# Optimization experiments

Hardware: AMD Instinct MI355X
Metric: run time of the kernel (lower is better)

Reference implementation:

```python
import jax, jax.numpy as jnp
import numpy as np

# dims: B=32 batch, F=40 max_frames, NB=36 num_boxes, R=512 region size, H=512 hidden
# feat_size D = R + 2H = 1536 ; relation attn input = 2D = 3072

def _soft_attention(feats, hidden, Wf, bf, Wh, bh, wa):
    # feats: (N, L, Din), hidden: (N, H) -> att feat (N, Din), alpha (N, L)
    e = jnp.tanh(feats @ Wf.T + bf + (hidden @ Wh.T + bh)[:, None, :]) @ wa  # (N, L)
    alpha = jax.nn.softmax(e, axis=1)
    att = jnp.einsum('nl,nld->nd', alpha, feats)
    return att, alpha


def setup_inputs() -> dict:
    key = jax.random.key(0)
    ks = jax.random.split(key, 16)
    B, F, NB, R, H = 32, 40, 36, 512, 512
    D = R + 2 * H  # 1536
    s = 0.02
    inp = {
        'i3d_feats': jax.random.normal(ks[0], (B, F, 2 * H), jnp.float32),
        'object_feats': jax.random.normal(ks[1], (B, F, NB, R), jnp.float32),
        'hidden_state': jax.random.normal(ks[2], (B, H), jnp.float32),
        # spatial SoftAttention(R, H, H)
        'Ws_f': jax.random.normal(ks[3], (H, R), jnp.float32) * s,
        'bs_f': jnp.zeros((H,), jnp.float32),
        'Ws_h': jax.random.normal(ks[4], (H, H), jnp.float32) * s,
        'bs_h': jnp.zeros((H,), jnp.float32),
        'was': jax.random.normal(ks[5], (H,), jnp.float32) * s,
        # relation SoftAttention(2D, H, H)
        'Wr_f': jax.random.normal(ks[6], (H, 2 * D), jnp.float32) * s,
        'br_f': jnp.zeros((H,), jnp.float32),
        'Wr_h': jax.random.normal(ks[7], (H, H), jnp.float32) * s,
        'br_h': jnp.zeros((H,), jnp.float32),
        'war': jax.random.normal(ks[8], (H,), jnp.float32) * s,
    }
    return inp


def reference(i3d_feats, object_feats, hidden_state,
              Ws_f, bs_f, Ws_h, bs_h, was,
              Wr_f, br_f, Wr_h, br_h, war):
    B, F, NB, R = object_feats.shape
    # ---- spatial attention over boxes (per frame) ----
    feats = object_feats.reshape(B * F, NB, R)
    hidden_rep = jnp.repeat(hidden_state, F, axis=0)  # == hidden.repeat(1,F).reshape(B*F,-1)
    obj_att, _ = _soft_attention(feats, hidden_rep, Ws_f, bs_f, Ws_h, bs_h, was)
    obj_att = obj_att.reshape(B, F, R)
    feat = jnp.concatenate([obj_att, i3d_feats], axis=-1)  # (B, F, D)
    D = feat.shape[-1]
    # ---- relation attention over all F*F frame pairs ----
    # pairwise[b, i*F + j] = concat(feat[b, j], feat[b, i])  (feat1 varies fast, feat2 slow)
    # Decompose Wr_f @ concat(fj, fi) = Wr1 @ fj + Wr2 @ fi to avoid O(F^2 * 2D) tensor.
    Wr1, Wr2 = Wr_f[:, :D], Wr_f[:, D:]
    p1 = feat @ Wr1.T  # (B, F, H), applied to fast index j
    p2 = feat @ Wr2.T  # (B, F, H), applied to slow index i
    hproj = hidden_state @ Wr_h.T + br_h  # (B, H)
    e = jnp.tanh(p2[:, :, None, :] + p1[:, None, :, :] + (hproj + br_f)[:, None, None, :]) @ war  # (B,F,F) [i,j]
    alpha = jax.nn.softmax(e.reshape(B, F * F), axis=1).reshape(B, F, F)
    # weighted sum of concat(feat[j], feat[i]) splits into two marginal sums
    rel1 = jnp.einsum('bij,bjd->bd', alpha, feat)
    rel2 = jnp.einsum('bij,bid->bd', alpha, feat)
    return jnp.concatenate([rel1, rel2], axis=-1)  # (B, 2D)
```

## Files before the change

### kernel.cpp

```cpp
#include <hip/hip_runtime.h>
#include <stdint.h>

#define B_SZ 32
#define F_SZ 40
#define NB_SZ 36
#define R_SZ 512
#define H_SZ 512
#define D_SZ 1536
#define M1 (B_SZ * F_SZ * NB_SZ)
#define NROW (B_SZ * F_SZ)
#define FNB (F_SZ * NB_SZ)

typedef __attribute__((ext_vector_type(8))) short short8;
typedef __attribute__((ext_vector_type(4))) float f32x4;

__device__ __forceinline__ unsigned short f2bf(float f) {
    unsigned int x = __float_as_uint(f);
    return (unsigned short)((x + 0x7fffu + ((x >> 16) & 1u)) >> 16);
}
__device__ __forceinline__ float bf2f(unsigned short u) {
    union { unsigned int i; float f; } v; v.i = ((unsigned int)u) << 16; return v.f;
}
__device__ __forceinline__ unsigned int cvtpk(float lo, float hi) {
    unsigned int r;
    asm("v_cvt_pk_bf16_f32 %0, %1, %2" : "=v"(r) : "v"(lo), "v"(hi));
    return r;
}
__device__ __forceinline__ float fast_rcp(float x) {
    float r; asm("v_rcp_f32 %0, %1" : "=v"(r) : "v"(x)); return r;
}
__device__ __forceinline__ float fast_tanh(float x) {
    float cx = fminf(fmaxf(x, -9.0f), 9.0f);
    float e = __expf(2.0f * cx);
    return (e - 1.0f) * fast_rcp(e + 1.0f);
}

__device__ __forceinline__ void gload_lds16(const void* gsrc, void* ldst) {
    __builtin_amdgcn_global_load_lds(
        (const __attribute__((address_space(1))) unsigned int*)gsrc,
        (__attribute__((address_space(3))) unsigned int*)ldst, 16, 0, 0);
}

__global__ __launch_bounds__(256) void k_pre(
    const float* __restrict__ hidden,
    const float* __restrict__ Wsh, const float* __restrict__ bsh,
    const float* __restrict__ bsf,
    const float* __restrict__ Wrh, const float* __restrict__ brh,
    const float* __restrict__ brf,
    float* __restrict__ hs, float* __restrict__ hr,
    const float* __restrict__ Wsf, unsigned short* __restrict__ Wsb)
{
    const int t = threadIdx.x;
    if (blockIdx.x >= 256) {
        int i = ((blockIdx.x - 256) * 256 + t) * 8;
        float4 f0 = *(const float4*)(Wsf + i);
        float4 f1 = *(const float4*)(Wsf + i + 4);
        uint4 pk = {cvtpk(f0.x, f0.y), cvtpk(f0.z, f0.w),
                    cvtpk(f1.x, f1.y), cvtpk(f1.z, f1.w)};
        *(uint4*)(Wsb + i) = pk;
        return;
    }
    __shared__ float hid[H_SZ];
    const int b = blockIdx.x >> 3, hc = blockIdx.x & 7;
    for (int i = t; i < H_SZ; i += 256) hid[i] = hidden[b * H_SZ + i];
    __syncthreads();
    const int h = hc * 64 + (t >> 2), kq = t & 3;
    const float* r1 = Wsh + (size_t)h * H_SZ + kq * 128;
    const float* r2 = Wrh + (size_t)h * H_SZ + kq * 128;
    const float* hh = hid + kq * 128;
    float a1 = 0.f, a2 = 0.f;
    for (int k = 0; k < 128; k += 4) {
        float4 v1 = *(const float4*)(r1 + k);
        float4 v2 = *(const float4*)(r2 + k);
        a1 += hh[k] * v1.x + hh[k+1] * v1.y + hh[k+2] * v1.z + hh[k+3] * v1.w;
        a2 += hh[k] * v2.x + hh[k+1] * v2.y + hh[k+2] * v2.z + hh[k+3] * v2.w;
    }
    a1 += __shfl_xor(a1, 1); a1 += __shfl_xor(a1, 2);
    a2 += __shfl_xor(a2, 1); a2 += __shfl_xor(a2, 2);
    if (kq == 0) {
        hs[b * H_SZ + h] = a1 + bsh[h] + bsf[h];
        hr[b * H_SZ + h] = a2 + brh[h] + brf[h];
    }
}

__global__ __launch_bounds__(256) void k_e1_mfma(
    const float* __restrict__ feats,
    const unsigned short* __restrict__ Wsb,
    const float* __restrict__ was,
    const float* __restrict__ hs,
    float* __restrict__ e1p)
{
    __shared__ __align__(16) unsigned char As[2][128 * 128];
    __shared__ __align__(16) unsigned char Bs[2][128 * 128];
    __shared__ float hsl[2 * 128];
    __shared__ float wasl[128];
    __shared__ float eps[2][128];

    const int bx = blockIdx.x;
    const int wid = (bx & 7) * 180 + (bx >> 3);
    const int mb = wid >> 2, by = wid & 3;
    const int m0 = mb * 128, hb = by * 128;
    const int t = threadIdx.x;
    const int b0 = m0 / FNB, b1 = (m0 + 127) / FNB;
    const int thr = (b0 + 1) * FNB - m0;

    if (t < 128) {
        hsl[t]       = hs[b0 * H_SZ + hb + t];
        hsl[128 + t] = hs[b1 * H_SZ + hb + t];
        wasl[t]      = was[hb + t];
    }

    const int lane = t & 63, w = t >> 6;
    const int wr = w >> 1, wc = w & 1;
    const int l15 = lane & 15, lk = lane >> 4;

    int ar[4], brw[4];
#pragma unroll
    for (int i = 0; i < 4; i++) {
        ar[i]  = wr * 64 + i * 16 + l15;
        brw[i] = wc * 64 + i * 16 + l15;
    }

    const int srow = t >> 3;
    const int scol = t & 7;
    const int wub  = (t & 192) * 16;

    float4 alo[4], ahi[4];
    f32x4 acc[4][4] = {};
    float ep[4][4] = {{0.f}};

#define E1_LOAD_A(K0) do { \
    _Pragma("unroll") \
    for (int it = 0; it < 4; it++) { \
        int r = it * 32 + srow; \
        const float* src = feats + (size_t)(m0 + r) * R_SZ + (K0) + scol * 8; \
        alo[it] = *(const float4*)src; \
        ahi[it] = *(const float4*)(src + 4); \
    } } while (0)

#define E1_STAGE_B(BUF, K0) do { \
    _Pragma("unroll") \
    for (int it = 0; it < 4; it++) { \
        int r = it * 32 + srow; \
        int gc = scol ^ (r & 7); \
        gload_lds16(Wsb + (size_t)(hb + r) * R_SZ + (K0) + gc * 8, \
                    &Bs[BUF][it * 4096 + wub]); \
    } } while (0)

#define E1_WRITE_A(BUF) do { \
    _Pragma("unroll") \
    for (int it = 0; it < 4; it++) { \
        int r = it * 32 + srow; \
        uint4 pk = {cvtpk(alo[it].x, alo[it].y), cvtpk(alo[it].z, alo[it].w), \
                    cvtpk(ahi[it].x, ahi[it].y), cvtpk(ahi[it].z, ahi[it].w)}; \
        *(uint4*)(&As[BUF][r * 128 + ((scol ^ (r & 7)) << 4)]) = pk; \
    } } while (0)

#define E1_COMPUTE(BUF) do { \
    _Pragma("unroll") \
    for (int ks = 0; ks < 2; ks++) { \
        short8 a[4], bv[4]; \
        int c = ks * 4 + lk; \
        _Pragma("unroll") \
        for (int i = 0; i < 4; i++) { \
            a[i]  = *(const short8*)(&As[BUF][ar[i]  * 128 + ((c ^ (ar[i]  & 7)) << 4)]); \
            bv[i] = *(const short8*)(&Bs[BUF][brw[i] * 128 + ((c ^ (brw[i] & 7)) << 4)]); \
        } \
        _Pragma("unroll") \
        for (int i = 0; i < 4; i++) \
        _Pragma("unroll") \
        for (int j = 0; j < 4; j++) \
            acc[i][j] = __builtin_amdgcn_mfma_f32_16x16x32_bf16(a[i], bv[j], acc[i][j], 0, 0, 0); \
    } } while (0)

    E1_LOAD_A(0);
    E1_STAGE_B(0, 0);
    E1_WRITE_A(0);
    __syncthreads();

    for (int ki = 0; ki < 8; ki++) {
        int cur = ki & 1, nxt = cur ^ 1;
        if (ki < 7) {
            E1_LOAD_A((ki + 1) * 64);
            E1_STAGE_B(nxt, (ki + 1) * 64);
        }
        E1_COMPUTE(cur);
        if (ki < 7) E1_WRITE_A(nxt);
        __syncthreads();
    }

#pragma unroll
    for (int j = 0; j < 4; j++) {
        int hl = wc * 64 + j * 16 + l15;
        float wv = wasl[hl];
#pragma unroll
        for (int i = 0; i < 4; i++) {
#pragma unroll
            for (int q = 0; q < 4; q++) {
                int r = wr * 64 + i * 16 + lk * 4 + q;
                float hv = hsl[(r >= thr ? 128 : 0) + hl];
                ep[i][q] += fast_tanh(acc[i][j][q] + hv) * wv;
            }
        }
    }
#pragma unroll
    for (int i = 0; i < 4; i++)
#pragma unroll
        for (int q = 0; q < 4; q++) {
            float v = ep[i][q];
            v += __shfl_xor(v, 1);
            v += __shfl_xor(v, 2);
            v += __shfl_xor(v, 4);
            v += __shfl_xor(v, 8);
            if (l15 == 0) eps[wc][wr * 64 + i * 16 + lk * 4 + q] = v;
        }
    __syncthreads();
    if (t < 128) e1p[(size_t)by * M1 + m0 + t] = eps[0][t] + eps[1][t];
#undef E1_LOAD_A
#undef E1_STAGE_B
#undef E1_WRITE_A
#undef E1_COMPUTE
}

__global__ __launch_bounds__(256) void k_softatt(
    const float* __restrict__ feats,
    const float* __restrict__ i3d,
    const float* __restrict__ e1p,
    unsigned short* __restrict__ feat)
{
    __shared__ float alpha[NB_SZ];
    const int n = blockIdx.x, t = threadIdx.x;
    if (t < 64) {
        float v = -1e30f;
        if (t < NB_SZ) {
            int idx = n * NB_SZ + t;
            v = e1p[idx] + e1p[M1 + idx] + e1p[2 * M1 + idx] + e1p[3 * M1 + idx];
        }
        float m = v;
#pragma unroll
        for (int off = 32; off; off >>= 1) m = fmaxf(m, __shfl_xor(m, off));
        float ex = (t < NB_SZ) ? expf(v - m) : 0.f;
        float ssum = ex;
#pragma unroll
        for (int off = 32; off; off >>= 1) ssum += __shfl_xor(ssum, off);
        if (t < NB_SZ) alpha[t] = ex / ssum;
    }
    __syncthreads();

    float a0 = 0.f, a1 = 0.f;
    const float* base = feats + (size_t)n * NB_SZ * R_SZ;
    for (int ll = 0; ll < NB_SZ; ll++) {
        float al = alpha[ll];
        float2 pv = *(const float2*)(base + ll * R_SZ + 2 * t);
        a0 += al * pv.x;
        a1 += al * pv.y;
    }
    feat[(size_t)n * D_SZ + 2 * t]     = f2bf(a0);
    feat[(size_t)n * D_SZ + 2 * t + 1] = f2bf(a1);
    float4 iv = *(const float4*)(i3d + (size_t)n * 1024 + t * 4);
    unsigned short o[4] = {f2bf(iv.x), f2bf(iv.y), f2bf(iv.z), f2bf(iv.w)};
    *(uint2*)(feat + (size_t)n * D_SZ + 512 + t * 4) = *(const uint2*)o;
}

__global__ __launch_bounds__(256) void k_pgemm_mfma(
    const unsigned short* __restrict__ feat,
    const float* __restrict__ Wrf,
    float* __restrict__ p)
{
    __shared__ __align__(16) unsigned char As[2][64 * 128];
    __shared__ __align__(16) unsigned char Bs[2][32 * 128];

    const int bx = blockIdx.x;
    const int wid = (bx & 7) * 80 + (bx >> 3);
    const int mb = wid % 20, nb = wid / 20;
    const int m0 = mb * 64, j0 = nb * 32;
    const int t = threadIdx.x;

    const int lane = t & 63, w = t >> 6;
    const int wr = w >> 1, wc = w & 1;
    const int l15 = lane & 15, lk = lane >> 4;

    const int srow = t >> 3;
    const int scol = t & 7;
    const int wub  = (t & 192) * 16;

    const size_t brow_base = (j0 < 512) ? (size_t)j0 * 3072
                                        : ((size_t)(j0 - 512) * 3072 + 1536);

    int ar[2];
    ar[0] = wr * 32 + l15; ar[1] = ar[0] + 16;
    const int brow = wc * 16 + l15;

    float4 blo, bhi;
    f32x4 acc[2] = {};

#define PG_STAGE_A(BUF, K0) do { \
    _Pragma("unroll") \
    for (int it = 0; it < 2; it++) { \
        int r = it * 32 + srow; \
        int gc = scol ^ (r & 7); \
        gload_lds16(feat + (size_t)(m0 + r) * D_SZ + (K0) + gc * 8, \
                    &As[BUF][it * 4096 + wub]); \
    } } while (0)

#define PG_LOAD_B(K0) do { \
    const float* src = Wrf + brow_base + (size_t)srow * 3072 + (K0) + scol * 8; \
    blo = *(const float4*)src; \
    bhi = *(const float4*)(src + 4); \
    } while (0)

#define PG_WRITE_B(BUF) do { \
    uint4 pk = {cvtpk(blo.x, blo.y), cvtpk(blo.z, blo.w), \
                cvtpk(bhi.x, bhi.y), cvtpk(bhi.z, bhi.w)}; \
    *(uint4*)(&Bs[BUF][srow * 128 + ((scol ^ (srow & 7)) << 4)]) = pk; \
    } while (0)

#define PG_COMPUTE(BUF) do { \
    _Pragma("unroll") \
    for (int ks = 0; ks < 2; ks++) { \
        int c = ks * 4 + lk; \
        short8 a0 = *(const short8*)(&As[BUF][ar[0] * 128 + ((c ^ (ar[0] & 7)) << 4)]); \
        short8 a1 = *(const short8*)(&As[BUF][ar[1] * 128 + ((c ^ (ar[1] & 7)) << 4)]); \
        short8 bv = *(const short8*)(&Bs[BUF][brow  * 128 + ((c ^ (brow  & 7)) << 4)]); \
        acc[0] = __builtin_amdgcn_mfma_f32_16x16x32_bf16(a0, bv, acc[0], 0, 0, 0); \
        acc[1] = __builtin_amdgcn_mfma_f32_16x16x32_bf16(a1, bv, acc[1], 0, 0, 0); \
    } } while (0)

    PG_LOAD_B(0);
    PG_STAGE_A(0, 0);
    PG_WRITE_B(0);
    __syncthreads();

    for (int ki = 0; ki < 24; ki++) {
        int cur = ki & 1, nxt = cur ^ 1;
        if (ki < 23) {
            PG_LOAD_B((ki + 1) * 64);
            PG_STAGE_A(nxt, (ki + 1) * 64);
        }
        PG_COMPUTE(cur);
        if (ki < 23) PG_WRITE_B(nxt);
        __syncthreads();
    }

#pragma unroll
    for (int i = 0; i < 2; i++)
#pragma unroll
        for (int q = 0; q < 4; q++) {
            int row = m0 + wr * 32 + i * 16 + lk * 4 + q;
            int col = j0 + wc * 16 + l15;
            p[(size_t)row * 1024 + col] = acc[i][q];
        }
#undef PG_STAGE_A
#undef PG_LOAD_B
#undef PG_WRITE_B
#undef PG_COMPUTE
}

__global__ __launch_bounds__(256) void k_e2(
    const float* __restrict__ p,
    const float* __restrict__ hr,
    const float* __restrict__ war,
    float* __restrict__ e2)
{
    const int blk = blockIdx.x;
    const int b = blk / F_SZ, i = blk % F_SZ;
    const int t = threadIdx.x;
    const int w = t >> 6, l = t & 63;
    const int ni = b * F_SZ + i;

    float base[8], warf[8];
    {
        float4 pa = *(const float4*)(p + (size_t)ni * 1024 + 512 + l * 8);
        float4 pb = *(const float4*)(p + (size_t)ni * 1024 + 512 + l * 8 + 4);
        float4 ha = *(const float4*)(hr + b * H_SZ + l * 8);
        float4 hb = *(const float4*)(hr + b * H_SZ + l * 8 + 4);
        base[0] = pa.x + ha.x; base[1] = pa.y + ha.y; base[2] = pa.z + ha.z; base[3] = pa.w + ha.w;
        base[4] = pb.x + hb.x; base[5] = pb.y + hb.y; base[6] = pb.z + hb.z; base[7] = pb.w + hb.w;
        float4 wa = *(const float4*)(war + l * 8);
        float4 wb = *(const float4*)(war + l * 8 + 4);
        warf[0] = wa.x; warf[1] = wa.y; warf[2] = wa.z; warf[3] = wa.w;
        warf[4] = wb.x; warf[5] = wb.y; warf[6] = wb.z; warf[7] = wb.w;
    }

    for (int j = w; j < F_SZ; j += 4) {
        const float* p1r = p + (size_t)(b * F_SZ + j) * 1024;
        float4 va = *(const float4*)(p1r + l * 8);
        float4 vb = *(const float4*)(p1r + l * 8 + 4);
        float pv[8] = {va.x, va.y, va.z, va.w, vb.x, vb.y, vb.z, vb.w};
        float s = 0.f;
#pragma unroll
        for (int u = 0; u < 8; u++) s += fast_tanh(pv[u] + base[u]) * warf[u];
#pragma unroll
        for (int off = 32; off; off >>= 1) s += __shfl_xor(s, off);
        if (l == 0) e2[(size_t)b * 1600 + i * F_SZ + j] = s;
    }
}

__global__ __launch_bounds__(256) void k_out(
    const float* __restrict__ e2,
    const unsigned short* __restrict__ feat,
    float* __restrict__ out)
{
    __shared__ float alpha[1600];
    __shared__ float red[4];
    __shared__ float rs[F_SZ], cs[F_SZ];
    const int b = blockIdx.x, t = threadIdx.x;
    const int w = t >> 6, l = t & 63;

    float lm = -1e30f;
    for (int idx = t; idx < 1600; idx += 256) {
        float v = e2[(size_t)b * 1600 + idx];
        alpha[idx] = v;
        lm = fmaxf(lm, v);
    }
#pragma unroll
    for (int off = 32; off; off >>= 1) lm = fmaxf(lm, __shfl_xor(lm, off));
    if (l == 0) red[w] = lm;
    __syncthreads();
    float M = fmaxf(fmaxf(red[0], red[1]), fmaxf(red[2], red[3]));
    __syncthreads();
    float ls = 0.f;
    for (int idx = t; idx < 1600; idx += 256) {
        float ex = expf(alpha[idx] - M);
        alpha[idx] = ex;
        ls += ex;
    }
#pragma unroll
    for (int off = 32; off; off >>= 1) ls += __shfl_xor(ls, off);
    if (l == 0) red[w] = ls;
    __syncthreads();
    float inv = 1.f / (red[0] + red[1] + red[2] + red[3]);

    if (t < F_SZ) {
        float s = 0.f;
        for (int j = 0; j < F_SZ; j++) s += alpha[t * F_SZ + j];
        rs[t] = s * inv;
    } else if (t >= 128 && t < 128 + F_SZ) {
        int j = t - 128;
        float s = 0.f;
        for (int i2 = 0; i2 < F_SZ; i2++) s += alpha[i2 * F_SZ + j];
        cs[j] = s * inv;
    }
    __syncthreads();

    float a1[6] = {0.f,0.f,0.f,0.f,0.f,0.f};
    float a2[6] = {0.f,0.f,0.f,0.f,0.f,0.f};
    for (int r = 0; r < F_SZ; r++) {
        float w1 = cs[r], w2 = rs[r];
        const unsigned short* fr = feat + (size_t)(b * F_SZ + r) * D_SZ;
#pragma unroll
        for (int u = 0; u < 6; u++) {
            float f = bf2f(fr[t + u * 256]);
            a1[u] += w1 * f;
            a2[u] += w2 * f;
        }
    }
#pragma unroll
    for (int u = 0; u < 6; u++) {
        out[(size_t)b * 3072 + t + u * 256]        = a1[u];
        out[(size_t)b * 3072 + 1536 + t + u * 256] = a2[u];
    }
}

extern "C" void kernel_launch(void* const* d_in, const int* in_sizes, int n_in,
                              void* d_out, int out_size, void* d_ws, size_t ws_size,
                              hipStream_t stream) {
    const float* i3d    = (const float*)d_in[0];
    const float* objf   = (const float*)d_in[1];
    const float* hidden = (const float*)d_in[2];
    const float* Wsf    = (const float*)d_in[3];
    const float* bsf    = (const float*)d_in[4];
    const float* Wsh    = (const float*)d_in[5];
    const float* bsh    = (const float*)d_in[6];
    const float* was    = (const float*)d_in[7];
    const float* Wrf    = (const float*)d_in[8];
    const float* brf    = (const float*)d_in[9];
    const float* Wrh    = (const float*)d_in[10];
    const float* brh    = (const float*)d_in[11];
    const float* war    = (const float*)d_in[12];
    float* out = (float*)d_out;

    char* ws = (char*)d_ws;
    float* hs  = (float*)(ws);
    float* hr  = (float*)(ws + 65536);
    float* p   = (float*)(ws + 131072);
    float* e1p = (float*)(ws + 131072);
    unsigned short* Wsb = (unsigned short*)(ws + 4849664);
    float* e2  = (float*)(ws + 5373952);
    unsigned short* feat = (unsigned short*)(ws + 5578752);

    k_pre<<<dim3(384), dim3(256), 0, stream>>>(hidden, Wsh, bsh, bsf, Wrh, brh, brf, hs, hr, Wsf, Wsb);
    k_e1_mfma<<<dim3(1440), dim3(256), 0, stream>>>(objf, Wsb, was, hs, e1p);
    k_softatt<<<dim3(NROW), dim3(256), 0, stream>>>(objf, i3d, e1p, feat);
    k_pgemm_mfma<<<dim3(640), dim3(256), 0, stream>>>(feat, Wrf, p);
    k_e2<<<dim3(NROW), dim3(256), 0, stream>>>(p, hr, war, e2);
    k_out<<<dim3(B_SZ), dim3(256), 0, stream>>>(e2, feat, out);
}
```

Measured before the change: 284.7 us.

## Retile relation GEMM, stage p1 in LDS for e2, split output, cheaper tanh

Several independent changes are bundled. The relation GEMM moves to 32x32 tiles with K=128 steps and twice the blocks. The e2 kernel loads the per-batch p1 rows into LDS once and lets 8 waves each handle one frame i. The output kernel is split across two blocks per batch, and tanh is rewritten as an exp2 plus reciprocal form without clamping. The spatial GEMM's A operand drops to a single LDS buffer, which adds an extra barrier per K step in exchange for lower LDS use and possibly higher occupancy.

Result: no change. 288.0 us (+1.2%).

```diff
diff --git a/kernel.cpp b/kernel.cpp
--- a/kernel.cpp
+++ b/kernel.cpp
@@ -30,9 +30,8 @@
     float r; asm("v_rcp_f32 %0, %1" : "=v"(r) : "v"(x)); return r;
 }
 __device__ __forceinline__ float fast_tanh(float x) {
-    float cx = fminf(fmaxf(x, -9.0f), 9.0f);
-    float e = __expf(2.0f * cx);
-    return (e - 1.0f) * fast_rcp(e + 1.0f);
+    float t = __builtin_amdgcn_exp2f(2.8853900817779268f * x);
+    return 1.0f - 2.0f * fast_rcp(t + 1.0f);
 }
 
 __device__ __forceinline__ void gload_lds16(const void* gsrc, void* ldst) {
@@ -90,7 +89,7 @@
     const float* __restrict__ hs,
     float* __restrict__ e1p)
 {
-    __shared__ __align__(16) unsigned char As[2][128 * 128];
+    __shared__ __align__(16) unsigned char As[128 * 128];
     __shared__ __align__(16) unsigned char Bs[2][128 * 128];
     __shared__ float hsl[2 * 128];
     __shared__ float wasl[128];
@@ -147,13 +146,13 @@
                     &Bs[BUF][it * 4096 + wub]); \
     } } while (0)
 
-#define E1_WRITE_A(BUF) do { \
+#define E1_WRITE_A() do { \
     _Pragma("unroll") \
     for (int it = 0; it < 4; it++) { \
         int r = it * 32 + srow; \
         uint4 pk = {cvtpk(alo[it].x, alo[it].y), cvtpk(alo[it].z, alo[it].w), \
                     cvtpk(ahi[it].x, ahi[it].y), cvtpk(ahi[it].z, ahi[it].w)}; \
-        *(uint4*)(&As[BUF][r * 128 + ((scol ^ (r & 7)) << 4)]) = pk; \
+        *(uint4*)(&As[r * 128 + ((scol ^ (r & 7)) << 4)]) = pk; \
     } } while (0)
 
 #define E1_COMPUTE(BUF) do { \
@@ -163,7 +162,7 @@
         int c = ks * 4 + lk; \
         _Pragma("unroll") \
         for (int i = 0; i < 4; i++) { \
-            a[i]  = *(const short8*)(&As[BUF][ar[i]  * 128 + ((c ^ (ar[i]  & 7)) << 4)]); \
+            a[i]  = *(const short8*)(&As[ar[i] * 128 + ((c ^ (ar[i] & 7)) << 4)]); \
             bv[i] = *(const short8*)(&Bs[BUF][brw[i] * 128 + ((c ^ (brw[i] & 7)) << 4)]); \
         } \
         _Pragma("unroll") \
@@ -175,18 +174,22 @@
 
     E1_LOAD_A(0);
     E1_STAGE_B(0, 0);
-    E1_WRITE_A(0);
-    __syncthreads();
-
+    E1_WRITE_A();
+    __syncthreads();
+
+#pragma unroll
     for (int ki = 0; ki < 8; ki++) {
-        int cur = ki & 1, nxt = cur ^ 1;
+        const int cur = ki & 1;
         if (ki < 7) {
             E1_LOAD_A((ki + 1) * 64);
-            E1_STAGE_B(nxt, (ki + 1) * 64);
+            E1_STAGE_B(cur ^ 1, (ki + 1) * 64);
         }
         E1_COMPUTE(cur);
-        if (ki < 7) E1_WRITE_A(nxt);
         __syncthreads();
+        if (ki < 7) {
+            E1_WRITE_A();
+            __syncthreads();
+        }
     }
 
 #pragma unroll
@@ -267,63 +270,65 @@
     const float* __restrict__ Wrf,
     float* __restrict__ p)
 {
-    __shared__ __align__(16) unsigned char As[2][64 * 128];
-    __shared__ __align__(16) unsigned char Bs[2][32 * 128];
+    __shared__ __align__(16) unsigned char As[2][32 * 256];
+    __shared__ __align__(16) unsigned char Bs[2][32 * 256];
 
     const int bx = blockIdx.x;
-    const int wid = (bx & 7) * 80 + (bx >> 3);
-    const int mb = wid % 20, nb = wid / 20;
-    const int m0 = mb * 64, j0 = nb * 32;
+    const int wid = (bx & 7) * 160 + (bx >> 3);
+    const int mb = wid % 40, nb = wid / 40;
+    const int m0 = mb * 32, j0 = nb * 32;
     const int t = threadIdx.x;
 
     const int lane = t & 63, w = t >> 6;
-    const int wr = w >> 1, wc = w & 1;
+    const int wrm = w >> 1, wcn = w & 1;
     const int l15 = lane & 15, lk = lane >> 4;
 
-    const int srow = t >> 3;
-    const int scol = t & 7;
-    const int wub  = (t & 192) * 16;
+    const int arow = wrm * 16 + l15;
+    const int brow = wcn * 16 + l15;
 
     const size_t brow_base = (j0 < 512) ? (size_t)j0 * 3072
                                         : ((size_t)(j0 - 512) * 3072 + 1536);
 
-    int ar[2];
-    ar[0] = wr * 32 + l15; ar[1] = ar[0] + 16;
-    const int brow = wc * 16 + l15;
-
-    float4 blo, bhi;
-    f32x4 acc[2] = {};
+    float4 blo[2], bhi[2];
+    f32x4 acc = {};
 
 #define PG_STAGE_A(BUF, K0) do { \
     _Pragma("unroll") \
     for (int it = 0; it < 2; it++) { \
-        int r = it * 32 + srow; \
-        int gc = scol ^ (r & 7); \
+        int cid = it * 256 + t; \
+        int r = cid >> 4, c = cid & 15; \
+        int gc = c ^ (r & 7); \
         gload_lds16(feat + (size_t)(m0 + r) * D_SZ + (K0) + gc * 8, \
-                    &As[BUF][it * 4096 + wub]); \
+                    &As[BUF][it * 4096 + (t & 192) * 16]); \
     } } while (0)
 
 #define PG_LOAD_B(K0) do { \
-    const float* src = Wrf + brow_base + (size_t)srow * 3072 + (K0) + scol * 8; \
-    blo = *(const float4*)src; \
-    bhi = *(const float4*)(src + 4); \
-    } while (0)
+    _Pragma("unroll") \
+    for (int it = 0; it < 2; it++) { \
+        int cid = it * 256 + t; \
+        int r = cid >> 4, c = cid & 15; \
+        const float* src = Wrf + brow_base + (size_t)r * 3072 + (K0) + c * 8; \
+        blo[it] = *(const float4*)src; \
+        bhi[it] = *(const float4*)(src + 4); \
+    } } while (0)
 
 #define PG_WRITE_B(BUF) do { \
-    uint4 pk = {cvtpk(blo.x, blo.y), cvtpk(blo.z, blo.w), \
-                cvtpk(bhi.x, bhi.y), cvtpk(bhi.z, bhi.w)}; \
-    *(uint4*)(&Bs[BUF][srow * 128 + ((scol ^ (srow & 7)) << 4)]) = pk; \
-    } while (0)
+    _Pragma("unroll") \
+    for (int it = 0; it < 2; it++) { \
+        int cid = it * 256 + t; \
+        int r = cid >> 4, c = cid & 15; \
+        uint4 pk = {cvtpk(blo[it].x, blo[it].y), cvtpk(blo[it].z, blo[it].w), \
+                    cvtpk(bhi[it].x, bhi[it].y), cvtpk(bhi[it].z, bhi[it].w)}; \
+        *(uint4*)(&Bs[BUF][r * 256 + ((c ^ (r & 7)) << 4)]) = pk; \
+    } } while (0)
 
 #define PG_COMPUTE(BUF) do { \
     _Pragma("unroll") \
-    for (int ks = 0; ks < 2; ks++) { \
+    for (int ks = 0; ks < 4; ks++) { \
         int c = ks * 4 + lk; \
-        short8 a0 = *(const short8*)(&As[BUF][ar[0] * 128 + ((c ^ (ar[0] & 7)) << 4)]); \
-        short8 a1 = *(const short8*)(&As[BUF][ar[1] * 128 + ((c ^ (ar[1] & 7)) << 4)]); \
-        short8 bv = *(const short8*)(&Bs[BUF][brow  * 128 + ((c ^ (brow  & 7)) << 4)]); \
-        acc[0] = __builtin_amdgcn_mfma_f32_16x16x32_bf16(a0, bv, acc[0], 0, 0, 0); \
-        acc[1] = __builtin_amdgcn_mfma_f32_16x16x32_bf16(a1, bv, acc[1], 0, 0, 0); \
+        short8 av = *(const short8*)(&As[BUF][arow * 256 + ((c ^ (arow & 7)) << 4)]); \
+        short8 bv = *(const short8*)(&Bs[BUF][brow * 256 + ((c ^ (brow & 7)) << 4)]); \
+        acc = __builtin_amdgcn_mfma_f32_16x16x32_bf16(av, bv, acc, 0, 0, 0); \
     } } while (0)
 
     PG_LOAD_B(0);
@@ -331,43 +336,51 @@
     PG_WRITE_B(0);
     __syncthreads();
 
-    for (int ki = 0; ki < 24; ki++) {
-        int cur = ki & 1, nxt = cur ^ 1;
-        if (ki < 23) {
-            PG_LOAD_B((ki + 1) * 64);
-            PG_STAGE_A(nxt, (ki + 1) * 64);
+#pragma unroll
+    for (int ki = 0; ki < 12; ki++) {
+        const int cur = ki & 1;
+        if (ki < 11) {
+            PG_LOAD_B((ki + 1) * 128);
+            PG_STAGE_A(cur ^ 1, (ki + 1) * 128);
         }
         PG_COMPUTE(cur);
-        if (ki < 23) PG_WRITE_B(nxt);
+        if (ki < 11) PG_WRITE_B(cur ^ 1);
         __syncthreads();
     }
 
 #pragma unroll
-    for (int i = 0; i < 2; i++)
-#pragma unroll
-        for (int q = 0; q < 4; q++) {
-            int row = m0 + wr * 32 + i * 16 + lk * 4 + q;
-            int col = j0 + wc * 16 + l15;
-            p[(size_t)row * 1024 + col] = acc[i][q];
-        }
+    for (int q = 0; q < 4; q++) {
+        int row = m0 + wrm * 16 + lk * 4 + q;
+        int col = j0 + wcn * 16 + l15;
+        p[(size_t)row * 1024 + col] = acc[q];
+    }
 #undef PG_STAGE_A
 #undef PG_LOAD_B
 #undef PG_WRITE_B
 #undef PG_COMPUTE
 }
 
-__global__ __launch_bounds__(256) void k_e2(
+__global__ __launch_bounds__(512) void k_e2(
     const float* __restrict__ p,
     const float* __restrict__ hr,
     const float* __restrict__ war,
     float* __restrict__ e2)
 {
+    __shared__ float p1l[F_SZ][512];
     const int blk = blockIdx.x;
-    const int b = blk / F_SZ, i = blk % F_SZ;
+    const int b = blk / 5, io = blk % 5;
     const int t = threadIdx.x;
     const int w = t >> 6, l = t & 63;
+
+    for (int cid = t; cid < F_SZ * 64; cid += 512) {
+        int r = cid >> 6, c = cid & 63;
+        const float* src = p + (size_t)(b * F_SZ + r) * 1024 + c * 8;
+        *(float4*)&p1l[r][c * 8]     = *(const float4*)src;
+        *(float4*)&p1l[r][c * 8 + 4] = *(const float4*)(src + 4);
+    }
+
+    const int i = io * 8 + w;
     const int ni = b * F_SZ + i;
-
     float base[8], warf[8];
     {
         float4 pa = *(const float4*)(p + (size_t)ni * 1024 + 512 + l * 8);
@@ -381,11 +394,12 @@
         warf[0] = wa.x; warf[1] = wa.y; warf[2] = wa.z; warf[3] = wa.w;
         warf[4] = wb.x; warf[5] = wb.y; warf[6] = wb.z; warf[7] = wb.w;
     }
-
-    for (int j = w; j < F_SZ; j += 4) {
-        const float* p1r = p + (size_t)(b * F_SZ + j) * 1024;
-        float4 va = *(const float4*)(p1r + l * 8);
-        float4 vb = *(const float4*)(p1r + l * 8 + 4);
+    __syncthreads();
+
+    for (int j = 0; j < F_SZ; j++) {
+        const float* r = p1l[j];
+        float4 va = *(const float4*)(r + l * 8);
+        float4 vb = *(const float4*)(r + l * 8 + 4);
         float pv[8] = {va.x, va.y, va.z, va.w, vb.x, vb.y, vb.z, vb.w};
         float s = 0.f;
 #pragma unroll
@@ -404,7 +418,8 @@
     __shared__ float alpha[1600];
     __shared__ float red[4];
     __shared__ float rs[F_SZ], cs[F_SZ];
-    const int b = blockIdx.x, t = threadIdx.x;
+    const int b = blockIdx.x >> 1, half = blockIdx.x & 1;
+    const int t = threadIdx.x;
     const int w = t >> 6, l = t & 63;
 
     float lm = -1e30f;
@@ -443,22 +458,23 @@
     }
     __syncthreads();
 
-    float a1[6] = {0.f,0.f,0.f,0.f,0.f,0.f};
-    float a2[6] = {0.f,0.f,0.f,0.f,0.f,0.f};
+    const int cb = half * 768;
+    float a1[3] = {0.f, 0.f, 0.f};
+    float a2[3] = {0.f, 0.f, 0.f};
     for (int r = 0; r < F_SZ; r++) {
         float w1 = cs[r], w2 = rs[r];
-        const unsigned short* fr = feat + (size_t)(b * F_SZ + r) * D_SZ;
-#pragma unroll
-        for (int u = 0; u < 6; u++) {
+        const unsigned short* fr = feat + (size_t)(b * F_SZ + r) * D_SZ + cb;
+#pragma unroll
+        for (int u = 0; u < 3; u++) {
             float f = bf2f(fr[t + u * 256]);
             a1[u] += w1 * f;
             a2[u] += w2 * f;
         }
     }
 #pragma unroll
-    for (int u = 0; u < 6; u++) {
-        out[(size_t)b * 3072 + t + u * 256]        = a1[u];
-        out[(size_t)b * 3072 + 1536 + t + u * 256] = a2[u];
+    for (int u = 0; u < 3; u++) {
+        out[(size_t)b * 3072 + cb + t + u * 256]        = a1[u];
+        out[(size_t)b * 3072 + 1536 + cb + t + u * 256] = a2[u];
     }
 }
 
@@ -492,7 +508,7 @@
     k_pre<<<dim3(384), dim3(256), 0, stream>>>(hidden, Wsh, bsh, bsf, Wrh, brh, brf, hs, hr, Wsf, Wsb);
     k_e1_mfma<<<dim3(1440), dim3(256), 0, stream>>>(objf, Wsb, was, hs, e1p);
     k_softatt<<<dim3(NROW), dim3(256), 0, stream>>>(objf, i3d, e1p, feat);
-    k_pgemm_mfma<<<dim3(640), dim3(256), 0, stream>>>(feat, Wrf, p);
-    k_e2<<<dim3(NROW), dim3(256), 0, stream>>>(p, hr, war, e2);
-    k_out<<<dim3(B_SZ), dim3(256), 0, stream>>>(e2, feat, out);
-}
+    k_pgemm_mfma<<<dim3(1280), dim3(256), 0, stream>>>(feat, Wrf, p);
+    k_e2<<<dim3(160), dim3(512), 0, stream>>>(p, hr, war, e2);
+    k_out<<<dim3(64), dim3(256), 0, stream>>>(e2, feat, out);
+}
```
